# Kernel tuning notes

Hardware: AMD Instinct MI355X
Metric: run time of the kernel (lower is better)

Reference implementation:

```python
import jax, jax.numpy as jnp
import numpy as np

NB_VEC = 4  # module init arg nbVec
TEMP = 20.0  # distance temperature in exp(-d/20)


def setup_inputs() -> dict:
    key = jax.random.key(0)
    k1, k2 = jax.random.split(key)
    B, C, H, W = 16, 64, 256, 256
    x = jax.random.normal(k1, (B, C, H, W), dtype=jnp.float32)
    # stands in for torch.rand score init used when prior is None
    score_init = jax.random.uniform(k2, (B, H * W), dtype=jnp.float32)
    return {"x": x, "score_init": score_init}


def reference(x, score_init):
    B, C, H, W = x.shape
    N = H * W
    # [B, N, C] flattened spatial features
    xf = jnp.transpose(x, (0, 2, 3, 1)).reshape(B, N, C)
    batch = jnp.arange(B)
    score = score_init
    vecs, sims = [], []
    for _ in range(NB_VEC):
        ind = jnp.argmax(score, axis=1)                      # [B] greedy pick
        raw = xf[batch, ind]                                 # [B, C]
        d2 = jnp.sum((xf - raw[:, None, :]) ** 2, axis=-1)   # [B, N]
        # safe sqrt (distance is exactly 0 at the selected pixel)
        sim = jnp.exp(-jnp.sqrt(jnp.maximum(d2, 1e-12)) / TEMP)
        simNorm = sim / jnp.sum(sim, axis=1, keepdims=True)
        reprVec = jnp.einsum('bnc,bn->bc', xf, simNorm)      # softmax-weighted agg
        vecs.append(reprVec)
        sims.append(sim.reshape(B, 1, H, W))
        score = (1.0 - sim) * score                          # suppress nearby pts
    vecList = jnp.stack(vecs, axis=1)                        # [B, nbVec, C]
    simList = jnp.concatenate(sims, axis=1)                  # [B, nbVec, H, W]
    # selectedPos is only incremented in the onlySimSample branch; zeros here
    selectedPos = jnp.zeros((B, 1, H, W), dtype=x.dtype)
    return vecList, simList, selectedPos
```

## Files before the change

kernel.cpp:

```cpp
#include <hip/hip_runtime.h>

#define BB 16
#define CC 64
#define NN 65536
#define NBV 4


__global__ void k_init(const float* __restrict__ sc_in,
                       float* __restrict__ score,
                       float* __restrict__ sel_out) {
    int i = blockIdx.x * 256 + threadIdx.x;
    score[i] = sc_in[i];
    sel_out[i] = 0.f;
}

__global__ void k_argmax1(const float* __restrict__ score,
                          float* __restrict__ bval, int* __restrict__ bidx) {
    int b = blockIdx.y, blk = blockIdx.x, tid = threadIdx.x;
    const float* s = score + (size_t)b * NN + blk * 1024;
    float v = -1e30f; int vi = 0x7fffffff;
    #pragma unroll
    for (int k = 0; k < 4; k++) {
        int idx = k * 256 + tid;
        float xv = s[idx];
        if (xv > v) { v = xv; vi = blk * 1024 + idx; }
    }
    __shared__ float sv[256]; __shared__ int si[256];
    sv[tid] = v; si[tid] = vi;
    __syncthreads();
    for (int st = 128; st > 0; st >>= 1) {
        if (tid < st) {
            float ov = sv[tid + st]; int oi = si[tid + st];
            if (ov > sv[tid] || (ov == sv[tid] && oi < si[tid])) { sv[tid] = ov; si[tid] = oi; }
        }
        __syncthreads();
    }
    if (tid == 0) { bval[b * 64 + blk] = sv[0]; bidx[b * 64 + blk] = si[0]; }
}

__global__ __launch_bounds__(256, 2)
void k_iter(const float* __restrict__ x, float* __restrict__ score,
            const float* __restrict__ bval, const int* __restrict__ bidx,
            float* __restrict__ wpart, float* __restrict__ sspart,
            float* __restrict__ sim_out, int iter) {
    int b = blockIdx.y, blk = blockIdx.x, tid = threadIdx.x;
    int lane = tid & 63, wv = tid >> 6;
    __shared__ float raw_s[64];
    __shared__ float lw[4][64];
    __shared__ float ls[4];

    if (tid < 64) {
        float v = bval[b * 64 + tid]; int vi = bidx[b * 64 + tid];
        #pragma unroll
        for (int off = 32; off >= 1; off >>= 1) {
            float ov = __shfl_down(v, off, 64); int oi = __shfl_down(vi, off, 64);
            if (ov > v || (ov == v && oi < vi)) { v = ov; vi = oi; }
        }
        int ind = __shfl(vi, 0, 64);
        raw_s[tid] = x[((size_t)b * 64 + tid) * NN + ind];
    }
    __syncthreads();

    float acc[64];
    #pragma unroll
    for (int c = 0; c < 64; c++) acc[c] = 0.f;
    float ssacc = 0.f;

    const float* xb = x + (size_t)b * 64 * NN;
    #pragma unroll 1
    for (int p = 0; p < 4; p++) {
        int n = blk * 1024 + p * 256 + tid;
        float xv[64];
        #pragma unroll
        for (int c = 0; c < 64; c++) xv[c] = xb[(size_t)c * NN + n];
        float d2 = 0.f;
        #pragma unroll
        for (int c = 0; c < 64; c++) { float df = xv[c] - raw_s[c]; d2 = fmaf(df, df, d2); }
        float sim = expf(-sqrtf(fmaxf(d2, 1e-12f)) * (1.0f / 20.0f));
        sim_out[((size_t)(b * 4 + iter)) * NN + n] = sim;
        if (iter < 3) score[(size_t)b * NN + n] *= (1.0f - sim);
        ssacc += sim;
        #pragma unroll
        for (int c = 0; c < 64; c++) acc[c] = fmaf(sim, xv[c], acc[c]);
    }

    #pragma unroll
    for (int c = 0; c < 64; c++) {
        float v = acc[c];
        #pragma unroll
        for (int off = 32; off >= 1; off >>= 1) v += __shfl_down(v, off, 64);
        if (lane == 0) lw[wv][c] = v;
    }
    {
        float v = ssacc;
        #pragma unroll
        for (int off = 32; off >= 1; off >>= 1) v += __shfl_down(v, off, 64);
        if (lane == 0) ls[wv] = v;
    }
    __syncthreads();
    if (tid < 64)
        wpart[(((size_t)b * 64) + blk) * 64 + tid] = lw[0][tid] + lw[1][tid] + lw[2][tid] + lw[3][tid];
    if (tid == 64)
        sspart[b * 64 + blk] = ls[0] + ls[1] + ls[2] + ls[3];
}

__global__ void k_fin(const float* __restrict__ wpart, const float* __restrict__ sspart,
                      float* __restrict__ vec_out, int iter) {
    int b = blockIdx.x, tid = threadIdx.x;
    float w = 0.f;
    for (int blk = 0; blk < 64; blk++) w += wpart[(((size_t)b * 64) + blk) * 64 + tid];
    float ss = 0.f;
    for (int blk = 0; blk < 64; blk++) ss += sspart[b * 64 + blk];
    vec_out[(b * 4 + iter) * 64 + tid] = w / ss;
}

extern "C" void kernel_launch(void* const* d_in, const int* in_sizes, int n_in,
                              void* d_out, int out_size, void* d_ws, size_t ws_size,
                              hipStream_t stream) {
    const float* x = (const float*)d_in[0];
    const float* sc_in = (const float*)d_in[1];
    float* out = (float*)d_out;
    float* vec_out = out;
    float* sim_out = vec_out + (size_t)BB * 4 * CC;
    float* sel_out = sim_out + (size_t)BB * 4 * NN;

    float* ws = (float*)d_ws;
    float* score = ws;
    float* bval = ws + (size_t)BB * NN;
    int* bidx = (int*)(bval + BB * 64);
    float* wpart = bval + 2 * BB * 64;
    float* sspart = wpart + (size_t)BB * 64 * 64;

    k_init<<<dim3(BB * NN / 256), 256, 0, stream>>>(sc_in, score, sel_out);
    for (int it = 0; it < NBV; it++) {
        k_argmax1<<<dim3(64, BB), 256, 0, stream>>>(score, bval, bidx);
        k_iter<<<dim3(64, BB), 256, 0, stream>>>(x, score, bval, bidx, wpart, sspart, sim_out, it);
        k_fin<<<dim3(BB), 64, 0, stream>>>(wpart, sspart, vec_out, it);
    }
}
```

Baseline: 631.0 us.

## Fuse argmax into iteration kernel and split channels across waves

Removes the separate init kernel and per-iteration argmax kernels. Score is now read from the input on the first iteration, sel zeroing is folded into the single initial argmax pass, and each iteration block computes a per-block max of the updated score into double-buffered bval/bidx for the next iteration. Inside k_iter the 64 channels are split across 4 waves of 16, with partial distances combined through shared memory and a barrier per group. This cuts register pressure (occupancy hint raised to 4) and avoids re-reading score. In exchange it adds a __syncthreads per 64-pixel group.

Result: faster. 547.6 us (-13.2%).

```diff
diff --git a/kernel.cpp b/kernel.cpp
--- a/kernel.cpp
+++ b/kernel.cpp
@@ -4,20 +4,15 @@
 #define CC 64
 #define NN 65536
 #define NBV 4
+#define B64 (BB * 64)
 
 
-__global__ void k_init(const float* __restrict__ sc_in,
-                       float* __restrict__ score,
-                       float* __restrict__ sel_out) {
-    int i = blockIdx.x * 256 + threadIdx.x;
-    score[i] = sc_in[i];
-    sel_out[i] = 0.f;
-}
-
-__global__ void k_argmax1(const float* __restrict__ score,
-                          float* __restrict__ bval, int* __restrict__ bidx) {
+__global__ __launch_bounds__(256)
+void k_argmax1(const float* __restrict__ sc_in,
+               float* __restrict__ bval, int* __restrict__ bidx,
+               float* __restrict__ sel_out) {
     int b = blockIdx.y, blk = blockIdx.x, tid = threadIdx.x;
-    const float* s = score + (size_t)b * NN + blk * 1024;
+    const float* s = sc_in + (size_t)b * NN + blk * 1024;
     float v = -1e30f; int vi = 0x7fffffff;
     #pragma unroll
     for (int k = 0; k < 4; k++) {
@@ -25,6 +20,9 @@
         float xv = s[idx];
         if (xv > v) { v = xv; vi = blk * 1024 + idx; }
     }
+    size_t gt = ((size_t)(b * 64 + blk)) * 256 + tid;
+    #pragma unroll
+    for (int k = 0; k < 4; k++) sel_out[gt + (size_t)k * 262144] = 0.f;
     __shared__ float sv[256]; __shared__ int si[256];
     sv[tid] = v; si[tid] = vi;
     __syncthreads();
@@ -38,19 +36,21 @@
     if (tid == 0) { bval[b * 64 + blk] = sv[0]; bidx[b * 64 + blk] = si[0]; }
 }
 
-__global__ __launch_bounds__(256, 2)
-void k_iter(const float* __restrict__ x, float* __restrict__ score,
-            const float* __restrict__ bval, const int* __restrict__ bidx,
+__global__ __launch_bounds__(256, 4)
+void k_iter(const float* __restrict__ x, const float* __restrict__ score_in,
+            float* __restrict__ score_out,
+            float* __restrict__ bval, int* __restrict__ bidx,
             float* __restrict__ wpart, float* __restrict__ sspart,
             float* __restrict__ sim_out, int iter) {
     int b = blockIdx.y, blk = blockIdx.x, tid = threadIdx.x;
     int lane = tid & 63, wv = tid >> 6;
     __shared__ float raw_s[64];
-    __shared__ float lw[4][64];
-    __shared__ float ls[4];
+    __shared__ float d2p[2][4][64];
+
+    int rb = (iter & 1) * B64, wb = ((iter & 1) ^ 1) * B64;
 
     if (tid < 64) {
-        float v = bval[b * 64 + tid]; int vi = bidx[b * 64 + tid];
+        float v = bval[rb + b * 64 + tid]; int vi = bidx[rb + b * 64 + tid];
         #pragma unroll
         for (int off = 32; off >= 1; off >>= 1) {
             float ov = __shfl_down(v, off, 64); int oi = __shfl_down(vi, off, 64);
@@ -61,47 +61,71 @@
     }
     __syncthreads();
 
-    float acc[64];
+    const float* xb = x + ((size_t)b * 64 + wv * 16) * NN;
+    float raw[16];
     #pragma unroll
-    for (int c = 0; c < 64; c++) acc[c] = 0.f;
-    float ssacc = 0.f;
+    for (int j = 0; j < 16; j++) raw[j] = raw_s[wv * 16 + j];
+    float acc[16];
+    #pragma unroll
+    for (int j = 0; j < 16; j++) acc[j] = 0.f;
 
-    const float* xb = x + (size_t)b * 64 * NN;
+    const size_t sb = (size_t)b * NN;
+    const size_t simb = (size_t)(b * NBV + iter) * NN;
+    const int nbase = blk * 1024 + lane;
+    const bool w0 = (wv == 0), upd = (iter < 3);
+
+    float ssacc = 0.f, smax = -1e30f; int smaxi = 0;
+    float sc_next = (w0 && upd) ? score_in[sb + nbase] : 0.f;
+
     #pragma unroll 1
-    for (int p = 0; p < 4; p++) {
-        int n = blk * 1024 + p * 256 + tid;
-        float xv[64];
+    for (int g = 0; g < 16; g++) {
+        int n = nbase + g * 64;
+        float xv[16], d2 = 0.f;
         #pragma unroll
-        for (int c = 0; c < 64; c++) xv[c] = xb[(size_t)c * NN + n];
-        float d2 = 0.f;
+        for (int j = 0; j < 16; j++) xv[j] = xb[(size_t)j * NN + n];
+        float sc_cur = sc_next;
+        if (w0 && upd && g < 15) sc_next = score_in[sb + n + 64];
         #pragma unroll
-        for (int c = 0; c < 64; c++) { float df = xv[c] - raw_s[c]; d2 = fmaf(df, df, d2); }
-        float sim = expf(-sqrtf(fmaxf(d2, 1e-12f)) * (1.0f / 20.0f));
-        sim_out[((size_t)(b * 4 + iter)) * NN + n] = sim;
-        if (iter < 3) score[(size_t)b * NN + n] *= (1.0f - sim);
-        ssacc += sim;
+        for (int j = 0; j < 16; j++) { float df = xv[j] - raw[j]; d2 = fmaf(df, df, d2); }
+        d2p[g & 1][wv][lane] = d2;
+        __syncthreads();
+        float d2s = (d2p[g & 1][0][lane] + d2p[g & 1][1][lane]) +
+                    (d2p[g & 1][2][lane] + d2p[g & 1][3][lane]);
+        float sim = expf(-sqrtf(fmaxf(d2s, 1e-12f)) * 0.05f);
         #pragma unroll
-        for (int c = 0; c < 64; c++) acc[c] = fmaf(sim, xv[c], acc[c]);
+        for (int j = 0; j < 16; j++) acc[j] = fmaf(sim, xv[j], acc[j]);
+        if (w0) {
+            ssacc += sim;
+            sim_out[simb + n] = sim;
+            if (upd) {
+                float sc = sc_cur * (1.f - sim);
+                score_out[sb + n] = sc;
+                if (sc > smax) { smax = sc; smaxi = n; }
+            }
+        }
     }
 
     #pragma unroll
-    for (int c = 0; c < 64; c++) {
-        float v = acc[c];
+    for (int j = 0; j < 16; j++) {
+        float v = acc[j];
         #pragma unroll
         for (int off = 32; off >= 1; off >>= 1) v += __shfl_down(v, off, 64);
-        if (lane == 0) lw[wv][c] = v;
+        if (lane == 0) wpart[(((size_t)b * 64) + blk) * 64 + wv * 16 + j] = v;
     }
-    {
+    if (w0) {
         float v = ssacc;
         #pragma unroll
         for (int off = 32; off >= 1; off >>= 1) v += __shfl_down(v, off, 64);
-        if (lane == 0) ls[wv] = v;
+        if (lane == 0) sspart[b * 64 + blk] = v;
+        if (upd) {
+            #pragma unroll
+            for (int off = 32; off >= 1; off >>= 1) {
+                float ov = __shfl_down(smax, off, 64); int oi = __shfl_down(smaxi, off, 64);
+                if (ov > smax || (ov == smax && oi < smaxi)) { smax = ov; smaxi = oi; }
+            }
+            if (lane == 0) { bval[wb + b * 64 + blk] = smax; bidx[wb + b * 64 + blk] = smaxi; }
+        }
     }
-    __syncthreads();
-    if (tid < 64)
-        wpart[(((size_t)b * 64) + blk) * 64 + tid] = lw[0][tid] + lw[1][tid] + lw[2][tid] + lw[3][tid];
-    if (tid == 64)
-        sspart[b * 64 + blk] = ls[0] + ls[1] + ls[2] + ls[3];
 }
 
 __global__ void k_fin(const float* __restrict__ wpart, const float* __restrict__ sspart,
@@ -111,7 +135,7 @@
     for (int blk = 0; blk < 64; blk++) w += wpart[(((size_t)b * 64) + blk) * 64 + tid];
     float ss = 0.f;
     for (int blk = 0; blk < 64; blk++) ss += sspart[b * 64 + blk];
-    vec_out[(b * 4 + iter) * 64 + tid] = w / ss;
+    vec_out[(b * NBV + iter) * 64 + tid] = w / ss;
 }
 
 extern "C" void kernel_launch(void* const* d_in, const int* in_sizes, int n_in,
@@ -121,20 +145,21 @@
     const float* sc_in = (const float*)d_in[1];
     float* out = (float*)d_out;
     float* vec_out = out;
-    float* sim_out = vec_out + (size_t)BB * 4 * CC;
-    float* sel_out = sim_out + (size_t)BB * 4 * NN;
+    float* sim_out = vec_out + (size_t)BB * NBV * CC;
+    float* sel_out = sim_out + (size_t)BB * NBV * NN;
 
     float* ws = (float*)d_ws;
     float* score = ws;
     float* bval = ws + (size_t)BB * NN;
-    int* bidx = (int*)(bval + BB * 64);
-    float* wpart = bval + 2 * BB * 64;
+    int* bidx = (int*)(bval + 2 * B64);
+    float* wpart = bval + 4 * B64;
     float* sspart = wpart + (size_t)BB * 64 * 64;
 
-    k_init<<<dim3(BB * NN / 256), 256, 0, stream>>>(sc_in, score, sel_out);
+    k_argmax1<<<dim3(64, BB), 256, 0, stream>>>(sc_in, bval, bidx, sel_out);
     for (int it = 0; it < NBV; it++) {
-        k_argmax1<<<dim3(64, BB), 256, 0, stream>>>(score, bval, bidx);
-        k_iter<<<dim3(64, BB), 256, 0, stream>>>(x, score, bval, bidx, wpart, sspart, sim_out, it);
+        const float* s_in = (it == 0) ? sc_in : score;
+        k_iter<<<dim3(64, BB), 256, 0, stream>>>(x, s_in, score, bval, bidx,
+                                                 wpart, sspart, sim_out, it);
         k_fin<<<dim3(BB), 64, 0, stream>>>(wpart, sspart, vec_out, it);
     }
 }
```
